# Kernel optimization log

Measured on AMD Instinct MI355X. Metric: run time of the kernel, lower is better.

## Reference

```python
import jax, jax.numpy as jnp
import numpy as np

# pywt coif4 decomposition low-pass filter (24 taps)
COIF4_DEC_LO = np.array([
    -1.7849850030882614e-06, -3.2596802368833675e-06, 3.1229875865345646e-05,
    6.233903446100713e-05, -0.00025997455248771324, -0.0005890207562443383,
    0.0012665619292989445, 0.003751436157278457, -0.00565828668661072,
    -0.015211731527946259, 0.025082261844864097, 0.03933442712333749,
    -0.09622044203398798, -0.06662747426342504, 0.4343860564914685,
    0.782238930920499, 0.41530840703043026, -0.05607731331675481,
    -0.08126669968087875, 0.026682300156053072, 0.016068943964776348,
    -0.0073461663276420935, -0.0016294920126017326, 0.0008923136685823146],
    dtype=np.float32)
L = 24
G0 = jnp.asarray(COIF4_DEC_LO[::-1].copy())                                  # rec_lo
G1 = jnp.asarray((COIF4_DEC_LO * ((-1.0) ** np.arange(L))).astype(np.float32))  # rec_hi
SCALER = (1.0, 0.2, 0.4, 0.6, 0.8)


def _sfb1d_last(lo, hi, g0, g1):
    # synthesis filter bank along last axis, periodization mode (pytorch_wavelets sfb1d)
    n = lo.shape[-1]
    N = 2 * n
    lead = lo.shape[:-1]

    def tconv(x, g):
        # transposed conv stride 2: y[m] = sum_k x[k] g[m-2k]; len = 2n+L-2
        xb = x.reshape((-1, 1, n))
        k = g[::-1].reshape((1, 1, L))
        y = jax.lax.conv_general_dilated(
            xb, k, window_strides=(1,), padding=[(L - 1, L - 1)],
            lhs_dilation=(2,), dimension_numbers=('NCH', 'OIH', 'NCH'))
        return y.reshape(lead + (N + L - 2,))

    y = tconv(lo, g0) + tconv(hi, g1)
    y = y.at[..., :L - 2].add(y[..., N:N + L - 2])  # periodic wrap
    y = y[..., :N]
    return jnp.roll(y, 1 - L // 2, axis=-1)


def _sfb2d(ll, lh, hl, hh):
    sw = lambda a: jnp.swapaxes(a, -1, -2)
    lo = sw(_sfb1d_last(sw(ll), sw(lh), G0, G1))   # columns (H axis)
    hi = sw(_sfb1d_last(sw(hl), sw(hh), G0, G1))
    return _sfb1d_last(lo, hi, G0, G1)             # rows (W axis)


def idwt_transform(yl, yhs):
    ll = yl
    for h in yhs[::-1]:  # coarsest high-pass first
        lh, hl, hh = h[:, :, 0], h[:, :, 1], h[:, :, 2]
        ll = _sfb2d(ll, lh, hl, hh)
    return ll


def grid_sample_bilinear(plane, pts):
    # plane [C,H,W]; pts [n,2] (x,y) in [-1,1]; align_corners=True, border padding
    C, H, W = plane.shape
    x = jnp.clip((pts[:, 0] + 1.0) * 0.5 * (W - 1), 0.0, W - 1)
    y = jnp.clip((pts[:, 1] + 1.0) * 0.5 * (H - 1), 0.0, H - 1)
    x0 = jnp.floor(x).astype(jnp.int32)
    y0 = jnp.floor(y).astype(jnp.int32)
    x1 = jnp.minimum(x0 + 1, W - 1)
    y1 = jnp.minimum(y0 + 1, H - 1)
    wx = x - x0
    wy = y - y0
    v00 = plane[:, y0, x0]  # [C, n]
    v01 = plane[:, y0, x1]
    v10 = plane[:, y1, x0]
    v11 = plane[:, y1, x1]
    out = (v00 * (1 - wy) * (1 - wx) + v01 * (1 - wy) * wx
           + v10 * wy * (1 - wx) + v11 * wy * wx)
    return out.T  # [n, C]


def setup_inputs() -> dict:
    key = jax.random.key(0)
    k0, k1, k2, k3, k4 = jax.random.split(key, 5)
    F_, R, n_pts = 32, 1024, 1048576
    yl = jax.random.uniform(k0, (1, F_, R // 8, R // 8), jnp.float32, 0.1, 0.5)
    yh0 = jax.random.normal(k1, (1, F_, 3, R // 2, R // 2), jnp.float32) * 0.05
    yh1 = jax.random.normal(k2, (1, F_, 3, R // 4, R // 4), jnp.float32) * 0.05
    yh2 = jax.random.normal(k3, (1, F_, 3, R // 8, R // 8), jnp.float32) * 0.05
    pts = jax.random.uniform(k4, (n_pts, 2), jnp.float32, -1.0, 1.0)
    return {"pts": pts, "yl": yl, "yh0": yh0, "yh1": yh1, "yh2": yh2}


def reference(pts, yl, yh0, yh1, yh2):
    yl_s = SCALER[0] * yl
    yhs = [SCALER[1] * yh0, SCALER[2] * yh1, SCALER[3] * yh2]
    plane = idwt_transform(yl_s, yhs)              # [1, F, R, R]
    feature = grid_sample_bilinear(plane[0], pts)  # [n, F]
    return feature.reshape(-1, plane.shape[1])
```

## Files before the change

### kernel.cpp

```cpp
#include <hip/hip_runtime.h>
#include <hip/hip_bf16.h>
#include <hip/hip_fp16.h>

constexpr int L = 24;
__device__ __constant__ float DEC_LO[L] = {
    -1.7849850030882614e-06f, -3.2596802368833675e-06f, 3.1229875865345646e-05f,
    6.233903446100713e-05f, -0.00025997455248771324f, -0.0005890207562443383f,
    0.0012665619292989445f, 0.003751436157278457f, -0.00565828668661072f,
    -0.015211731527946259f, 0.025082261844864097f, 0.03933442712333749f,
    -0.09622044203398798f, -0.06662747426342504f, 0.4343860564914685f,
    0.782238930920499f, 0.41530840703043026f, -0.05607731331675481f,
    -0.08126669968087875f, 0.026682300156053072f, 0.016068943964776348f,
    -0.0073461663276420935f, -0.0016294920126017326f, 0.0008923136685823146f
};

__device__ __forceinline__ float g0f(int m) { return DEC_LO[23 - m]; }
__device__ __forceinline__ float g1f(int m) { return (m & 1) ? -DEC_LO[m] : DEC_LO[m]; }

__global__ void colpass2_kernel(const float* __restrict__ lowA, const float* __restrict__ highA,
                                float sLA, float sHA, int lACS, int hACS,
                                const float* __restrict__ lowB, const float* __restrict__ highB,
                                float sLB, float sHB, int lBCS, int hBCS,
                                int n, int W,
                                float* __restrict__ outA, float* __restrict__ outB)
{
    int x = blockIdx.x * 64 + threadIdx.x;
    int q = blockIdx.y * blockDim.y + threadIdx.y;
    int z = blockIdx.z;
    int c = z & 31;
    bool isB = z >= 32;
    const float* low  = isB ? lowB  : lowA;
    const float* high = isB ? highB : highA;
    float sLow  = isB ? sLB : sLA;
    float sHigh = isB ? sHB : sHA;
    int lowCS  = isB ? lBCS : lACS;
    int highCS = isB ? hBCS : hACS;
    float* out = isB ? outB : outA;

    int mask = n - 1;
    const float* lp = low + (size_t)c * lowCS + x;
    const float* hp = high + (size_t)c * highCS + x;
    float a0 = 0.f, a1 = 0.f;
#pragma unroll
    for (int s = 0; s <= 12; ++s) {
        int r = (q + 6 - s) & mask;
        float lv = sLow * lp[(size_t)r * W];
        float hv = sHigh * hp[(size_t)r * W];
        if (s >= 1)  a0 = fmaf(g0f(2 * s - 1), lv, fmaf(g1f(2 * s - 1), hv, a0));
        if (s <= 11) a1 = fmaf(g0f(2 * s), lv, fmaf(g1f(2 * s), hv, a1));
    }
    size_t ob = ((size_t)c * (2 * n) + 2 * q) * W + x;
    out[ob] = a0;
    out[ob + W] = a1;
}

__global__ void rowpass_kernel(const float* __restrict__ lo, const float* __restrict__ hi,
                               int n, float* __restrict__ out)
{
    int q = blockIdx.x * 64 + threadIdx.x;
    int y = blockIdx.y * blockDim.y + threadIdx.y;
    int c = blockIdx.z;
    int N = 2 * n, mask = n - 1;
    const float* lp = lo + ((size_t)c * N + y) * n;
    const float* hp = hi + ((size_t)c * N + y) * n;
    float a0 = 0.f, a1 = 0.f;
#pragma unroll
    for (int s = 0; s <= 12; ++s) {
        int r = (q + 6 - s) & mask;
        float lv = lp[r];
        float hv = hp[r];
        if (s >= 1)  a0 = fmaf(g0f(2 * s - 1), lv, fmaf(g1f(2 * s - 1), hv, a0));
        if (s <= 11) a1 = fmaf(g0f(2 * s), lv, fmaf(g1f(2 * s), hv, a1));
    }
    float2* op = (float2*)(out + ((size_t)c * N + y) * N + 2 * q);
    *op = make_float2(a0, a1);
}

__global__ void colpass4h2_kernel(const float4* __restrict__ loA, const float4* __restrict__ hiA,
                                  float sLA, float sHA, int lACS4, int hACS4,
                                  const float4* __restrict__ loB, const float4* __restrict__ hiB,
                                  float sLB, float sHB, int lBCS4, int hBCS4,
                                  __half* __restrict__ outA, __half* __restrict__ outB)
{
    const int mask = 511, W4 = 128;
    int x = blockIdx.x * 64 + threadIdx.x;
    int q0 = (blockIdx.y * 4 + threadIdx.y) * 4;
    int z = blockIdx.z;
    int c = z & 31;
    bool isB = z >= 32;
    const float4* lo = isB ? loB : loA;
    const float4* hi = isB ? hiB : hiA;
    float sLow  = isB ? sLB : sLA;
    float sHigh = isB ? sHB : sHA;
    int loCS4 = isB ? lBCS4 : lACS4;
    int hiCS4 = isB ? hBCS4 : hACS4;
    __half* out = isB ? outB : outA;

    const float4* lp = lo + (size_t)c * loCS4 + x;
    const float4* hp = hi + (size_t)c * hiCS4 + x;

    float4 a0[4], a1[4];
#pragma unroll
    for (int j = 0; j < 4; ++j) {
        a0[j] = make_float4(0.f, 0.f, 0.f, 0.f);
        a1[j] = make_float4(0.f, 0.f, 0.f, 0.f);
    }

#pragma unroll
    for (int ro = 0; ro < 16; ++ro) {
        int r = (q0 - 6 + ro) & mask;
        float4 lv = lp[(size_t)r * W4];
        float4 hv = hp[(size_t)r * W4];
        lv.x *= sLow;  lv.y *= sLow;  lv.z *= sLow;  lv.w *= sLow;
        hv.x *= sHigh; hv.y *= sHigh; hv.z *= sHigh; hv.w *= sHigh;
#pragma unroll
        for (int j = 0; j < 4; ++j) {
            int s = j + 12 - ro;
            if (s >= 1 && s <= 12) {
                float gl = g0f(2 * s - 1), gh = g1f(2 * s - 1);
                a0[j].x = fmaf(gl, lv.x, fmaf(gh, hv.x, a0[j].x));
                a0[j].y = fmaf(gl, lv.y, fmaf(gh, hv.y, a0[j].y));
                a0[j].z = fmaf(gl, lv.z, fmaf(gh, hv.z, a0[j].z));
                a0[j].w = fmaf(gl, lv.w, fmaf(gh, hv.w, a0[j].w));
            }
            if (s >= 0 && s <= 11) {
                float gl = g0f(2 * s), gh = g1f(2 * s);
                a1[j].x = fmaf(gl, lv.x, fmaf(gh, hv.x, a1[j].x));
                a1[j].y = fmaf(gl, lv.y, fmaf(gh, hv.y, a1[j].y));
                a1[j].z = fmaf(gl, lv.z, fmaf(gh, hv.z, a1[j].z));
                a1[j].w = fmaf(gl, lv.w, fmaf(gh, hv.w, a1[j].w));
            }
        }
    }

#pragma unroll
    for (int j = 0; j < 4; ++j) {
        size_t ob = ((size_t)c * 1024 + 2 * (q0 + j)) * 512 + 4 * x;
        __half2 p0 = __floats2half2_rn(a0[j].x, a0[j].y), p1 = __floats2half2_rn(a0[j].z, a0[j].w);
        __half2 p2 = __floats2half2_rn(a1[j].x, a1[j].y), p3 = __floats2half2_rn(a1[j].z, a1[j].w);
        *(uint2*)&out[ob]       = make_uint2(*(unsigned int*)&p0, *(unsigned int*)&p1);
        *(uint2*)&out[ob + 512] = make_uint2(*(unsigned int*)&p2, *(unsigned int*)&p3);
    }
}

__global__ void rowpass16_hwc_kernel(const __half* __restrict__ lo, const __half* __restrict__ hi,
                                     __half* __restrict__ out)
{
    const int n = 512, N = 1024, mask = 511;
    int y = blockIdx.y;
    int qb = blockIdx.x * 64;
    int t = threadIdx.x;
    int c = t >> 3;
    int tq = t & 7;
    int q0 = qb + tq * 8;

    const __half* lp = lo + ((size_t)c * N + y) * n;
    const __half* hp = hi + ((size_t)c * N + y) * n;

    float wlo[24], whi[24];
#pragma unroll
    for (int k = 0; k < 3; ++k) {
        int s0 = (q0 - 8 + 8 * k) & mask;
        float4 vl = *(const float4*)(lp + s0);
        float4 vh = *(const float4*)(hp + s0);
        const __half2* hl = (const __half2*)&vl;
        const __half2* hh = (const __half2*)&vh;
#pragma unroll
        for (int j = 0; j < 4; ++j) {
            float2 fl = __half22float2(hl[j]);
            float2 fh = __half22float2(hh[j]);
            wlo[k * 8 + 2 * j]     = fl.x;
            wlo[k * 8 + 2 * j + 1] = fl.y;
            whi[k * 8 + 2 * j]     = fh.x;
            whi[k * 8 + 2 * j + 1] = fh.y;
        }
    }

    __shared__ __half tile[128][34];

#pragma unroll
    for (int j = 0; j < 8; ++j) {
        float a0 = 0.f, a1 = 0.f;
#pragma unroll
        for (int s = 0; s <= 12; ++s) {
            int li = j + 14 - s;
            float lv = wlo[li];
            float hv = whi[li];
            if (s >= 1)  a0 = fmaf(g0f(2 * s - 1), lv, fmaf(g1f(2 * s - 1), hv, a0));
            if (s <= 11) a1 = fmaf(g0f(2 * s), lv, fmaf(g1f(2 * s), hv, a1));
        }
        int pl = 16 * tq + 2 * j;
        tile[pl][c]     = __float2half_rn(a0);
        tile[pl + 1][c] = __float2half_rn(a1);
    }
    __syncthreads();

    int p = t >> 1;
    int c0 = (t & 1) * 16;
    unsigned int w[8];
#pragma unroll
    for (int k = 0; k < 8; ++k) {
        unsigned int l16 = __half_as_ushort(tile[p][c0 + 2 * k]);
        unsigned int h16 = __half_as_ushort(tile[p][c0 + 2 * k + 1]);
        w[k] = l16 | (h16 << 16);
    }
    size_t ob = ((size_t)y * 1024 + 2 * qb + p) * 32 + c0;
    *(uint4*)&out[ob]       = make_uint4(w[0], w[1], w[2], w[3]);
    *(uint4*)(&out[ob + 8]) = make_uint4(w[4], w[5], w[6], w[7]);
}

struct alignas(16) HV { __half2 h[4]; };

__global__ __launch_bounds__(256) void sample_kernel(const float* __restrict__ pts,
                                                     const __half* __restrict__ plane,
                                                     float* __restrict__ out, int npts)
{
    int tid = blockIdx.x * 256 + threadIdx.x;
    int p = tid >> 1;
    int cg = (tid & 1) * 16;
    float2 pt = *(const float2*)(pts + 2 * p);
    float xf = fminf(fmaxf((pt.x + 1.f) * 0.5f * 1023.f, 0.f), 1023.f);
    float yf = fminf(fmaxf((pt.y + 1.f) * 0.5f * 1023.f, 0.f), 1023.f);
    int x0 = (int)xf, y0 = (int)yf;
    int x1 = min(x0 + 1, 1023), y1 = min(y0 + 1, 1023);
    float wx = xf - (float)x0, wy = yf - (float)y0;
    size_t r0 = (size_t)y0 * 1024, r1 = (size_t)y1 * 1024;
    const __half* base = plane + cg;
    HV v00a = *(const HV*)(base + (r0 + x0) * 32);
    HV v00b = *(const HV*)(base + (r0 + x0) * 32 + 8);
    HV v01a = *(const HV*)(base + (r0 + x1) * 32);
    HV v01b = *(const HV*)(base + (r0 + x1) * 32 + 8);
    HV v10a = *(const HV*)(base + (r1 + x0) * 32);
    HV v10b = *(const HV*)(base + (r1 + x0) * 32 + 8);
    HV v11a = *(const HV*)(base + (r1 + x1) * 32);
    HV v11b = *(const HV*)(base + (r1 + x1) * 32 + 8);

    float o[16];
#pragma unroll
    for (int k = 0; k < 4; ++k) {
        float2 f00 = __half22float2(v00a.h[k]);
        float2 f01 = __half22float2(v01a.h[k]);
        float2 f10 = __half22float2(v10a.h[k]);
        float2 f11 = __half22float2(v11a.h[k]);
        o[2 * k]     = (f00.x * (1.f - wx) + f01.x * wx) * (1.f - wy)
                     + (f10.x * (1.f - wx) + f11.x * wx) * wy;
        o[2 * k + 1] = (f00.y * (1.f - wx) + f01.y * wx) * (1.f - wy)
                     + (f10.y * (1.f - wx) + f11.y * wx) * wy;
    }
#pragma unroll
    for (int k = 0; k < 4; ++k) {
        float2 f00 = __half22float2(v00b.h[k]);
        float2 f01 = __half22float2(v01b.h[k]);
        float2 f10 = __half22float2(v10b.h[k]);
        float2 f11 = __half22float2(v11b.h[k]);
        o[8 + 2 * k]     = (f00.x * (1.f - wx) + f01.x * wx) * (1.f - wy)
                         + (f10.x * (1.f - wx) + f11.x * wx) * wy;
        o[8 + 2 * k + 1] = (f00.y * (1.f - wx) + f01.y * wx) * (1.f - wy)
                         + (f10.y * (1.f - wx) + f11.y * wx) * wy;
    }
    float* ob = out + (size_t)p * 32 + cg;
    *(float4*)ob        = make_float4(o[0], o[1], o[2], o[3]);
    *(float4*)(ob + 4)  = make_float4(o[4], o[5], o[6], o[7]);
    *(float4*)(ob + 8)  = make_float4(o[8], o[9], o[10], o[11]);
    *(float4*)(ob + 12) = make_float4(o[12], o[13], o[14], o[15]);
}

extern "C" void kernel_launch(void* const* d_in, const int* in_sizes, int n_in,
                              void* d_out, int out_size, void* d_ws, size_t ws_size,
                              hipStream_t stream)
{
    const float* pts = (const float*)d_in[0];
    const float* yl  = (const float*)d_in[1];
    const float* yh0 = (const float*)d_in[2];
    const float* yh1 = (const float*)d_in[3];
    const float* yh2 = (const float*)d_in[4];
    const int npts = in_sizes[0] / 2;

    char* ws = (char*)d_ws;
    float*  llbuf    = (float*)ws;
    float*  tmpA     = (float*)(ws + 33554432);
    float*  tmpB     = (float*)(ws + 67108864);
    __half* tmpAh    = (__half*)(ws + 33554432);
    __half* tmpBh    = (__half*)(ws + 67108864);
    __half* planeHWC = (__half*)(ws + 100663296);

    dim3 cb(64, 4, 1);

    {
        int n = 128, nn = n * n;
        dim3 cg(n / 64, n / 4, 64);
        colpass2_kernel<<<cg, cb, 0, stream>>>(yl, yh2 + 0 * nn, 1.0f, 0.6f, nn, 3 * nn,
                                               yh2 + 1 * nn, yh2 + 2 * nn, 0.6f, 0.6f, 3 * nn, 3 * nn,
                                               n, n, tmpA, tmpB);
        dim3 rg(n / 64, (2 * n) / 4, 32);
        rowpass_kernel<<<rg, cb, 0, stream>>>(tmpA, tmpB, n, llbuf);
    }
    {
        int n = 256, nn = n * n;
        dim3 cg(n / 64, n / 4, 64);
        colpass2_kernel<<<cg, cb, 0, stream>>>(llbuf, yh1 + 0 * nn, 1.0f, 0.4f, nn, 3 * nn,
                                               yh1 + 1 * nn, yh1 + 2 * nn, 0.4f, 0.4f, 3 * nn, 3 * nn,
                                               n, n, tmpA, tmpB);
        dim3 rg(n / 64, (2 * n) / 4, 32);
        rowpass_kernel<<<rg, cb, 0, stream>>>(tmpA, tmpB, n, llbuf);
    }
    {
        int nn = 512 * 512;
        dim3 cg(2, 32, 64);
        colpass4h2_kernel<<<cg, cb, 0, stream>>>(
            (const float4*)llbuf, (const float4*)(yh0 + 0 * nn), 1.0f, 0.2f, nn / 4, 3 * nn / 4,
            (const float4*)(yh0 + 1 * nn), (const float4*)(yh0 + 2 * nn), 0.2f, 0.2f, 3 * nn / 4, 3 * nn / 4,
            tmpAh, tmpBh);
        dim3 rg(8, 1024);
        rowpass16_hwc_kernel<<<rg, 256, 0, stream>>>(tmpAh, tmpBh, planeHWC);
    }
    sample_kernel<<<(npts * 2) / 256, 256, 0, stream>>>(pts, planeHWC, (float*)d_out, npts);
}
```

Before: 254.3 us.

## Bin sample points by 32x32 plane tile before bilinear gather

Adds a counting sort of the query points by 32x32 tile of the output plane (histogram, scan, scatter), so the sample kernel reads sorted points and gathers plane texels with much better cache locality. The output is written back through a permutation index. Sample blocks are also swizzled across groups of eight. The cost is four extra launches, global atomics over 1M points with heavy contention on 1024 counters, extra point and perm traffic, and scattered output writes.

New measurement: 676.8 us. +166.1%, slower.

```diff
diff --git a/kernel.cpp b/kernel.cpp
--- a/kernel.cpp
+++ b/kernel.cpp
@@ -209,16 +209,68 @@
     *(uint4*)(&out[ob + 8]) = make_uint4(w[4], w[5], w[6], w[7]);
 }
 
+__device__ __forceinline__ int tile_of(float2 pt)
+{
+    float xf = fminf(fmaxf((pt.x + 1.f) * 0.5f * 1023.f, 0.f), 1023.f);
+    float yf = fminf(fmaxf((pt.y + 1.f) * 0.5f * 1023.f, 0.f), 1023.f);
+    int x0 = (int)xf, y0 = (int)yf;
+    return ((y0 >> 5) << 5) | (x0 >> 5);
+}
+
+__global__ void zero_kernel(unsigned int* __restrict__ cnt, unsigned int* __restrict__ off)
+{
+    cnt[threadIdx.x] = 0u;
+    off[threadIdx.x] = 0u;
+}
+
+__global__ void hist_kernel(const float2* __restrict__ pts, unsigned int* __restrict__ cnt)
+{
+    int i = blockIdx.x * 256 + threadIdx.x;
+    atomicAdd(&cnt[tile_of(pts[i])], 1u);
+}
+
+__global__ void scan_kernel(const unsigned int* __restrict__ cnt, unsigned int* __restrict__ off)
+{
+    __shared__ unsigned int s[1024];
+    int t = threadIdx.x;
+    unsigned int mine = cnt[t];
+    s[t] = mine;
+    __syncthreads();
+    for (int d = 1; d < 1024; d <<= 1) {
+        unsigned int v = (t >= d) ? s[t - d] : 0u;
+        __syncthreads();
+        s[t] += v;
+        __syncthreads();
+    }
+    off[t] = s[t] - mine;
+}
+
+__global__ void scatter_kernel(const float2* __restrict__ pts, unsigned int* __restrict__ off,
+                               unsigned int* __restrict__ perm, float2* __restrict__ ptsS)
+{
+    int i = blockIdx.x * 256 + threadIdx.x;
+    float2 pt = pts[i];
+    unsigned int pos = atomicAdd(&off[tile_of(pt)], 1u);
+    perm[pos] = (unsigned int)i;
+    ptsS[pos] = pt;
+}
+
 struct alignas(16) HV { __half2 h[4]; };
 
-__global__ __launch_bounds__(256) void sample_kernel(const float* __restrict__ pts,
+__global__ __launch_bounds__(256) void sample_kernel(const float2* __restrict__ ptsS,
+                                                     const unsigned int* __restrict__ perm,
                                                      const __half* __restrict__ plane,
-                                                     float* __restrict__ out, int npts)
-{
-    int tid = blockIdx.x * 256 + threadIdx.x;
-    int p = tid >> 1;
+                                                     float* __restrict__ out)
+{
+    int b = blockIdx.x;
+    int chunk = gridDim.x >> 3;
+    int swz = (b & 7) * chunk + (b >> 3);
+    int tid = swz * 256 + threadIdx.x;
+    int i = tid >> 1;
     int cg = (tid & 1) * 16;
-    float2 pt = *(const float2*)(pts + 2 * p);
+
+    float2 pt = ptsS[i];
+    unsigned int p = perm[i];
     float xf = fminf(fmaxf((pt.x + 1.f) * 0.5f * 1023.f, 0.f), 1023.f);
     float yf = fminf(fmaxf((pt.y + 1.f) * 0.5f * 1023.f, 0.f), 1023.f);
     int x0 = (int)xf, y0 = (int)yf;
@@ -283,8 +335,17 @@
     __half* tmpAh    = (__half*)(ws + 33554432);
     __half* tmpBh    = (__half*)(ws + 67108864);
     __half* planeHWC = (__half*)(ws + 100663296);
+    unsigned int* cnt  = (unsigned int*)(ws + 167772160);
+    unsigned int* off  = (unsigned int*)(ws + 167776256);
+    unsigned int* perm = (unsigned int*)(ws + 167780352);
+    float2*       ptsS = (float2*)(ws + 171974656);
 
     dim3 cb(64, 4, 1);
+
+    zero_kernel<<<1, 1024, 0, stream>>>(cnt, off);
+    hist_kernel<<<npts / 256, 256, 0, stream>>>((const float2*)pts, cnt);
+    scan_kernel<<<1, 1024, 0, stream>>>(cnt, off);
+    scatter_kernel<<<npts / 256, 256, 0, stream>>>((const float2*)pts, off, perm, ptsS);
 
     {
         int n = 128, nn = n * n;
@@ -314,5 +375,5 @@
         dim3 rg(8, 1024);
         rowpass16_hwc_kernel<<<rg, 256, 0, stream>>>(tmpAh, tmpBh, planeHWC);
     }
-    sample_kernel<<<(npts * 2) / 256, 256, 0, stream>>>(pts, planeHWC, (float*)d_out, npts);
-}
+    sample_kernel<<<(npts * 2) / 256, 256, 0, stream>>>(ptsS, perm, planeHWC, (float*)d_out);
+}
```

## Bin sample points by row band before bilinear gather for cache locality

Applied to the files above, without the earlier changes.

Adds a pre-pass that scatters query points into 16 horizontal row bands of the plane, recording a permutation, and then runs the sampler band by band. Blocks in a band gather from a small slice of the fp16 HWC plane, which is meant to improve L2 hit rates for the random bilinear gathers. In exchange it adds an atomic scatter pass, permuted non-coalesced output writes, and a fixed per-band capacity that assumes a roughly uniform point distribution.

New measurement: 334.3 us. 1.31x slower.

```diff
diff --git a/kernel.cpp b/kernel.cpp
--- a/kernel.cpp
+++ b/kernel.cpp
@@ -16,6 +16,9 @@
 
 __device__ __forceinline__ float g0f(int m) { return DEC_LO[23 - m]; }
 __device__ __forceinline__ float g1f(int m) { return (m & 1) ? -DEC_LO[m] : DEC_LO[m]; }
+
+#define BAND_CAP   67584
+#define BLK_PER_BD 528
 
 __global__ void colpass2_kernel(const float* __restrict__ lowA, const float* __restrict__ highA,
                                 float sLA, float sHA, int lACS, int hACS,
@@ -209,16 +212,52 @@
     *(uint4*)(&out[ob + 8]) = make_uint4(w[4], w[5], w[6], w[7]);
 }
 
+__global__ void zerocur_kernel(unsigned int* __restrict__ cursor)
+{
+    cursor[threadIdx.x] = 0u;
+}
+
+__global__ void scatter16_kernel(const float2* __restrict__ pts, unsigned int* __restrict__ cursor,
+                                 float2* __restrict__ ptsS, unsigned int* __restrict__ perm)
+{
+    __shared__ unsigned int lcnt[16], lbase[16];
+    int t = threadIdx.x;
+    if (t < 16) lcnt[t] = 0u;
+    __syncthreads();
+    int gid = blockIdx.x * 256 + t;
+    float2 pt = pts[gid];
+    float yf = fminf(fmaxf((pt.y + 1.f) * 0.5f * 1023.f, 0.f), 1023.f);
+    int band = ((int)yf) >> 6;
+    unsigned int rank = atomicAdd(&lcnt[band], 1u);
+    __syncthreads();
+    if (t < 16) lbase[t] = atomicAdd(&cursor[t * 16], lcnt[t]);
+    __syncthreads();
+    unsigned int dest = (unsigned int)band * BAND_CAP + lbase[band] + rank;
+    ptsS[dest] = pt;
+    perm[dest] = (unsigned int)gid;
+}
+
 struct alignas(16) HV { __half2 h[4]; };
 
-__global__ __launch_bounds__(256) void sample_kernel(const float* __restrict__ pts,
+__global__ __launch_bounds__(256) void sample_kernel(const float2* __restrict__ ptsS,
+                                                     const unsigned int* __restrict__ perm,
+                                                     const unsigned int* __restrict__ cursor,
                                                      const __half* __restrict__ plane,
-                                                     float* __restrict__ out, int npts)
-{
-    int tid = blockIdx.x * 256 + threadIdx.x;
-    int p = tid >> 1;
-    int cg = (tid & 1) * 16;
-    float2 pt = *(const float2*)(pts + 2 * p);
+                                                     float* __restrict__ out)
+{
+    int b = blockIdx.x;
+    int j = b & 7, s = b >> 3;
+    int band = j + 8 * (s / BLK_PER_BD);
+    int slot = s % BLK_PER_BD;
+    int t = threadIdx.x;
+    int pl = slot * 128 + (t >> 1);
+    unsigned int cnt = cursor[band * 16];
+    if ((unsigned int)pl >= cnt) return;
+    int i = band * BAND_CAP + pl;
+    int cg = (t & 1) * 16;
+
+    float2 pt = ptsS[i];
+    unsigned int p = perm[i];
     float xf = fminf(fmaxf((pt.x + 1.f) * 0.5f * 1023.f, 0.f), 1023.f);
     float yf = fminf(fmaxf((pt.y + 1.f) * 0.5f * 1023.f, 0.f), 1023.f);
     int x0 = (int)xf, y0 = (int)yf;
@@ -283,8 +322,14 @@
     __half* tmpAh    = (__half*)(ws + 33554432);
     __half* tmpBh    = (__half*)(ws + 67108864);
     __half* planeHWC = (__half*)(ws + 100663296);
+    unsigned int* cursor = (unsigned int*)(ws + 167772160);
+    float2*       ptsS   = (float2*)(ws + 167773184);
+    unsigned int* perm   = (unsigned int*)(ws + 176424960);
 
     dim3 cb(64, 4, 1);
+
+    zerocur_kernel<<<1, 256, 0, stream>>>(cursor);
+    scatter16_kernel<<<npts / 256, 256, 0, stream>>>((const float2*)pts, cursor, ptsS, perm);
 
     {
         int n = 128, nn = n * n;
@@ -314,5 +359,5 @@
         dim3 rg(8, 1024);
         rowpass16_hwc_kernel<<<rg, 256, 0, stream>>>(tmpAh, tmpBh, planeHWC);
     }
-    sample_kernel<<<(npts * 2) / 256, 256, 0, stream>>>(pts, planeHWC, (float*)d_out, npts);
-}
+    sample_kernel<<<16 * BLK_PER_BD, 256, 0, stream>>>(ptsS, perm, cursor, planeHWC, (float*)d_out);
+}
```
